# Optimization experiments

Measured on AMD Instinct MI355X. Metric: run time of the kernel, lower is better.

Reference implementation:

```python
import jax, jax.numpy as jnp
import numpy as np

EMBED_DIM = 1024
NUM_HEADS = 16
HEAD_DIM = EMBED_DIM // NUM_HEADS


def setup_inputs() -> dict:
    key = jax.random.key(0)
    ks = jax.random.split(key, 7)
    N, L = 2, 2048
    sv = 1.0 / np.sqrt(HEAD_DIM)
    so = 1.0 / np.sqrt(EMBED_DIM)
    return {
        "values": jax.random.normal(ks[0], (N, L, EMBED_DIM), jnp.float32),
        "keys": jax.random.normal(ks[1], (N, L, EMBED_DIM), jnp.float32),
        "query": jax.random.normal(ks[2], (N, L, EMBED_DIM), jnp.float32),
        # NOTE: original torch code applies self.values to v, k AND q; keys/queries
        # Linears are dead parameters, so only Wv/bv and fc_out are materialized.
        "Wv": jax.random.uniform(ks[3], (HEAD_DIM, HEAD_DIM), jnp.float32, -sv, sv),
        "bv": jax.random.uniform(ks[4], (HEAD_DIM,), jnp.float32, -sv, sv),
        "Wo": jax.random.uniform(ks[5], (EMBED_DIM, EMBED_DIM), jnp.float32, -so, so),
        "bo": jax.random.uniform(ks[6], (EMBED_DIM,), jnp.float32, -so, so),
    }


def reference(values, keys, query, Wv, bv, Wo, bo):
    N, Lq, _ = query.shape
    Lk = keys.shape[1]
    Lv = values.shape[1]
    # split heads: (N, L, H, D)
    v = values.reshape(N, Lv, NUM_HEADS, HEAD_DIM)
    k = keys.reshape(N, Lk, NUM_HEADS, HEAD_DIM)
    q = query.reshape(N, Lq, NUM_HEADS, HEAD_DIM)
    # faithful to source: the SAME value projection is applied to v, k, q
    proj = lambda x: jnp.einsum('nlhd,ed->nlhe', x, Wv) + bv
    v = proj(v)
    k = proj(k)
    q = proj(q)
    # energy: (N, H, Q, K); note scaling by sqrt(embed_dim), as in source
    energy = jnp.einsum('nqhd,nkhd->nhqk', q, k)
    attention = jax.nn.softmax(energy / jnp.sqrt(jnp.float32(EMBED_DIM)), axis=3)
    out = jnp.einsum('nhql,nlhd->nqhd', attention, v).reshape(N, Lq, EMBED_DIM)
    return out @ Wo.T + bo
```

## Files before the change

### kernel.cpp

```cpp
#include <hip/hip_runtime.h>

typedef unsigned short u16;
typedef __bf16 bf16x4 __attribute__((ext_vector_type(4)));
typedef __bf16 bf16x8 __attribute__((ext_vector_type(8)));
typedef float  f32x4  __attribute__((ext_vector_type(4)));
typedef float  f32x16 __attribute__((ext_vector_type(16)));

#define MFMA16(a, b, c) __builtin_amdgcn_mfma_f32_16x16x32_bf16((a), (b), (c), 0, 0, 0)
#define MFMA32(a, b, c) __builtin_amdgcn_mfma_f32_32x32x16_bf16((a), (b), (c), 0, 0, 0)


__global__ __launch_bounds__(256) void prep_kernel(
    const float* __restrict__ values, const float* __restrict__ keys,
    const float* __restrict__ query,  const float* __restrict__ Wv,
    const float* __restrict__ bv,     const float* __restrict__ Wo,
    u16* __restrict__ Qb, u16* __restrict__ Kb, u16* __restrict__ VTb,
    u16* __restrict__ Wob) {
    const int b = blockIdx.x;
    const int t = b >> 10;
    if (t == 3) {
        const int i = ((b - 3072) * 256 + threadIdx.x) * 4;
        float4 v = *(const float4*)&Wo[i];
        bf16x4 o = { (__bf16)v.x, (__bf16)v.y, (__bf16)v.z, (__bf16)v.w };
        *(bf16x4*)&Wob[i] = o;
        return;
    }
    __shared__ __align__(16) u16 Wvs[64 * 72];
    __shared__ __align__(16) u16 Xs[64 * 72];
    const int lt = b & 31, h = (b >> 5) & 15, n = (b >> 9) & 1;
    const int nh = n * 16 + h, l0 = lt * 64;
    const int tid = threadIdx.x, wave = tid >> 6, lane = tid & 63;
    const int quad = lane >> 4, l16 = lane & 15;
    const float* xin = (t == 0) ? values : (t == 1 ? keys : query);

#pragma unroll
    for (int j = 0; j < 4; ++j) {
        const int chunk = tid + 256 * j, r = chunk >> 4, c = (chunk & 15) * 4;
        float4 w = *(const float4*)&Wv[r * 64 + c];
        bf16x4 wb = { (__bf16)w.x, (__bf16)w.y, (__bf16)w.z, (__bf16)w.w };
        *(bf16x4*)&Wvs[r * 72 + c] = wb;
        float4 x = *(const float4*)&xin[(size_t)(n * 2048 + l0 + r) * 1024 + h * 64 + c];
        bf16x4 xb = { (__bf16)x.x, (__bf16)x.y, (__bf16)x.z, (__bf16)x.w };
        *(bf16x4*)&Xs[r * 72 + c] = xb;
    }
    __syncthreads();

    bf16x8 wf[4][2], xf[2];
#pragma unroll
    for (int f = 0; f < 4; ++f)
#pragma unroll
        for (int ks = 0; ks < 2; ++ks)
            wf[f][ks] = *(const bf16x8*)&Wvs[(f * 16 + l16) * 72 + ks * 32 + quad * 8];
#pragma unroll
    for (int ks = 0; ks < 2; ++ks)
        xf[ks] = *(const bf16x8*)&Xs[(wave * 16 + l16) * 72 + ks * 32 + quad * 8];

    f32x4 acc[4];
#pragma unroll
    for (int i = 0; i < 4; ++i) acc[i] = (f32x4){0.f, 0.f, 0.f, 0.f};

    if (t == 0) {
#pragma unroll
        for (int nf = 0; nf < 4; ++nf) {
            acc[nf] = MFMA16(xf[0], wf[nf][0], acc[nf]);
            acc[nf] = MFMA16(xf[1], wf[nf][1], acc[nf]);
        }
    } else {
#pragma unroll
        for (int mf = 0; mf < 4; ++mf) {
            acc[mf] = MFMA16(wf[mf][0], xf[0], acc[mf]);
            acc[mf] = MFMA16(wf[mf][1], xf[1], acc[mf]);
        }
    }
    __syncthreads();

    const float scale = (t == 2) ? 0.04508422f : 1.0f;
    if (t == 0) {
#pragma unroll
        for (int nf = 0; nf < 4; ++nf) {
            const float bias = bv[nf * 16 + l16];
            bf16x4 o = { (__bf16)(acc[nf][0] + bias), (__bf16)(acc[nf][1] + bias),
                         (__bf16)(acc[nf][2] + bias), (__bf16)(acc[nf][3] + bias) };
            *(bf16x4*)&Xs[(nf * 16 + l16) * 72 + wave * 16 + quad * 4] = o;
        }
    } else {
#pragma unroll
        for (int mf = 0; mf < 4; ++mf) {
            bf16x4 o = { (__bf16)((acc[mf][0] + bv[mf * 16 + quad * 4 + 0]) * scale),
                         (__bf16)((acc[mf][1] + bv[mf * 16 + quad * 4 + 1]) * scale),
                         (__bf16)((acc[mf][2] + bv[mf * 16 + quad * 4 + 2]) * scale),
                         (__bf16)((acc[mf][3] + bv[mf * 16 + quad * 4 + 3]) * scale) };
            *(bf16x4*)&Xs[(wave * 16 + l16) * 72 + mf * 16 + quad * 4] = o;
        }
    }
    __syncthreads();

    u16* dst = (t == 0) ? VTb : (t == 1 ? Kb : Qb);
#pragma unroll
    for (int j = 0; j < 2; ++j) {
        const int chunk = tid + 256 * j, r = chunk >> 3, c = (chunk & 7) * 8;
        const size_t off = (t == 0) ? (size_t)(nh * 64 + r) * 2048 + l0 + c
                                    : (size_t)(nh * 2048 + l0 + r) * 64 + c;
        *(int4*)&dst[off] = *(const int4*)&Xs[r * 72 + c];
    }
}

__global__ __launch_bounds__(256, 4) void flash_kernel(
    const u16* __restrict__ Qb, const u16* __restrict__ Kb,
    const u16* __restrict__ VTb, u16* __restrict__ Op,
    float* __restrict__ Lp) {
    __shared__ __align__(16) u16 Ks[64 * 72];
    __shared__ __align__(16) u16 Vs[64 * 72];
    __shared__ __align__(16) u16 Ps[4][32 * 72];
    const int b = blockIdx.x;
    const int nh = b >> 5, qsl = (b >> 1) & 15, ks = b & 1;
    const int tid = threadIdx.x, wave = tid >> 6, lane = tid & 63;
    const int l32 = lane & 31, half = lane >> 5;
    const int q0 = qsl * 128 + wave * 32;
    const int s4 = (b >> 1) * 4 + wave;
    u16* Pw = &Ps[wave][0];

    const u16* Qg = Qb + ((size_t)nh * 2048 + q0) * 64;
    bf16x8 qf[4];
#pragma unroll
    for (int kg = 0; kg < 4; ++kg)
        qf[kg] = *(const bf16x8*)&Qg[l32 * 64 + kg * 16 + half * 8];

    f32x16 Oacc[2];
#pragma unroll
    for (int dt = 0; dt < 2; ++dt)
#pragma unroll
        for (int r = 0; r < 16; ++r) Oacc[dt][r] = 0.f;
    float lsum = 0.f;

    const u16* Kg = Kb + (size_t)nh * 2048 * 64;
    const u16* Vg = VTb + (size_t)nh * 64 * 2048;

    for (int kt = 0; kt < 16; ++kt) {
        __syncthreads();
        const int k0 = ks * 1024 + kt * 64;
#pragma unroll
        for (int j = 0; j < 2; ++j) {
            const int chunk = tid + 256 * j, r = chunk >> 3, c = (chunk & 7) * 8;
            *(int4*)&Ks[r * 72 + c] = *(const int4*)&Kg[(size_t)(k0 + r) * 64 + c];
            *(int4*)&Vs[r * 72 + c] = *(const int4*)&Vg[(size_t)r * 2048 + k0 + c];
        }
        __syncthreads();

#pragma unroll
        for (int t2 = 0; t2 < 2; ++t2) {
            f32x16 s;
#pragma unroll
            for (int r = 0; r < 16; ++r) s[r] = 0.f;
#pragma unroll
            for (int kg = 0; kg < 4; ++kg) {
                bf16x8 ak = *(const bf16x8*)&Ks[(t2 * 32 + l32) * 72 + kg * 16 + half * 8];
                s = MFMA32(ak, qf[kg], s);
            }
#pragma unroll
            for (int a = 0; a < 4; ++a) {
                const float p0 = __builtin_amdgcn_exp2f(s[4 * a + 0]);
                const float p1 = __builtin_amdgcn_exp2f(s[4 * a + 1]);
                const float p2 = __builtin_amdgcn_exp2f(s[4 * a + 2]);
                const float p3 = __builtin_amdgcn_exp2f(s[4 * a + 3]);
                lsum += (p0 + p1) + (p2 + p3);
                bf16x4 pk = { (__bf16)p0, (__bf16)p1, (__bf16)p2, (__bf16)p3 };
                *(bf16x4*)&Pw[l32 * 72 + t2 * 32 + a * 8 + half * 4] = pk;
            }
        }

#pragma unroll
        for (int kk = 0; kk < 4; ++kk) {
            bf16x8 bp = *(const bf16x8*)&Pw[l32 * 72 + kk * 16 + half * 8];
#pragma unroll
            for (int dt = 0; dt < 2; ++dt) {
                bf16x8 av = *(const bf16x8*)&Vs[(dt * 32 + l32) * 72 + kk * 16 + half * 8];
                Oacc[dt] = MFMA32(av, bp, Oacc[dt]);
            }
        }
    }

    const float lq = lsum + __shfl_xor(lsum, 32);
    if (half == 0)
        Lp[((size_t)s4 * 2 + ks) * 32 + l32] = lq;

#pragma unroll
    for (int dt = 0; dt < 2; ++dt)
#pragma unroll
        for (int a = 0; a < 4; ++a) {
            bf16x4 o = { (__bf16)Oacc[dt][4 * a + 0], (__bf16)Oacc[dt][4 * a + 1],
                         (__bf16)Oacc[dt][4 * a + 2], (__bf16)Oacc[dt][4 * a + 3] };
            *(bf16x4*)&Pw[l32 * 72 + dt * 32 + a * 8 + half * 4] = o;
        }
    u16* Ob = Op + (size_t)ks * 4194304 +
              ((size_t)(nh >> 4) * 2048 + q0) * 1024 + (nh & 15) * 64;
#pragma unroll
    for (int j = 0; j < 4; ++j) {
        const int chunk = lane + 64 * j, r = chunk >> 3, c = (chunk & 7) * 8;
        *(int4*)&Ob[(size_t)r * 1024 + c] = *(const int4*)&Pw[r * 72 + c];
    }
}

__global__ __launch_bounds__(256) void combine_kernel(
    const u16* __restrict__ Op, const float* __restrict__ Lp,
    u16* __restrict__ AOb) {
    const int u = blockIdx.x * 256 + threadIdx.x;
    const int row = u >> 7, ecol = (u & 127) * 8;
    const int h = ecol >> 6;
    const int n = row >> 11, qsl = (row >> 7) & 15, w = (row >> 5) & 3, q = row & 31;
    const int s4 = (((n * 16 + h) * 16 + qsl) << 2) + w;
    const float l = Lp[(size_t)s4 * 2 * 32 + q] + Lp[((size_t)s4 * 2 + 1) * 32 + q];
    const float inv = 1.0f / l;
    const size_t off = (size_t)row * 1024 + ecol;
    bf16x8 a = *(const bf16x8*)&Op[off];
    bf16x8 c = *(const bf16x8*)&Op[4194304 + off];
    bf16x8 o;
#pragma unroll
    for (int i = 0; i < 8; ++i)
        o[i] = (__bf16)(((float)a[i] + (float)c[i]) * inv);
    *(bf16x8*)&AOb[off] = o;
}

__global__ __launch_bounds__(512) void out_gemm_kernel(
    const u16* __restrict__ A, const u16* __restrict__ Bw,
    const float* __restrict__ bo, float* __restrict__ out) {
    __shared__ __align__(16) u16 As[128 * 72];
    __shared__ __align__(16) u16 Bs[64 * 72];
    const int b = blockIdx.x, rt = b >> 4, ct = b & 15;
    const int row0 = rt * 128, col0 = ct * 64;
    const int tid = threadIdx.x, wave = tid >> 6, lane = tid & 63;
    const int l32 = lane & 31, half = lane >> 5;
    const int wr = wave & 3, wc = wave >> 2;

    f32x16 acc;
#pragma unroll
    for (int r = 0; r < 16; ++r) acc[r] = 0.f;

    for (int kt = 0; kt < 16; ++kt) {
        __syncthreads();
        const int k0 = kt * 64;
#pragma unroll
        for (int j = 0; j < 2; ++j) {
            const int chunk = tid + 512 * j, r = chunk >> 3, c = (chunk & 7) * 8;
            *(int4*)&As[r * 72 + c] = *(const int4*)&A[(size_t)(row0 + r) * 1024 + k0 + c];
        }
        {
            const int r = tid >> 3, c = (tid & 7) * 8;
            *(int4*)&Bs[r * 72 + c] = *(const int4*)&Bw[(size_t)(col0 + r) * 1024 + k0 + c];
        }
        __syncthreads();
#pragma unroll
        for (int kg = 0; kg < 4; ++kg) {
            bf16x8 af = *(const bf16x8*)&As[(wr * 32 + l32) * 72 + kg * 16 + half * 8];
            bf16x8 bf = *(const bf16x8*)&Bs[(wc * 32 + l32) * 72 + kg * 16 + half * 8];
            acc = MFMA32(af, bf, acc);
        }
    }

    const int col = col0 + wc * 32 + l32;
    const float bias = bo[col];
#pragma unroll
    for (int r = 0; r < 16; ++r) {
        const int row = row0 + wr * 32 + (r & 3) + 8 * (r >> 2) + 4 * half;
        out[(size_t)row * 1024 + col] = acc[r] + bias;
    }
}

extern "C" void kernel_launch(void* const* d_in, const int* in_sizes, int n_in,
                              void* d_out, int out_size, void* d_ws, size_t ws_size,
                              hipStream_t stream) {
    (void)in_sizes; (void)n_in; (void)out_size; (void)ws_size;
    const float* values = (const float*)d_in[0];
    const float* keys   = (const float*)d_in[1];
    const float* query  = (const float*)d_in[2];
    const float* Wv     = (const float*)d_in[3];
    const float* bv     = (const float*)d_in[4];
    const float* Wo     = (const float*)d_in[5];
    const float* bo     = (const float*)d_in[6];

    char* ws = (char*)d_ws;
    u16*   Qb  = (u16*)(ws);
    u16*   Kb  = (u16*)(ws + (8ull  << 20));
    u16*   VTb = (u16*)(ws + (16ull << 20));
    u16*   AOb = (u16*)(ws + (24ull << 20));
    u16*   Wob = (u16*)(ws + (32ull << 20));
    u16*   Op  = (u16*)(ws + (34ull << 20));
    float* Lp  = (float*)(ws + (50ull << 20));

    prep_kernel<<<4096, 256, 0, stream>>>(values, keys, query, Wv, bv, Wo,
                                          Qb, Kb, VTb, Wob);
    flash_kernel<<<1024, 256, 0, stream>>>(Qb, Kb, VTb, Op, Lp);
    combine_kernel<<<2048, 256, 0, stream>>>(Op, Lp, AOb);
    out_gemm_kernel<<<512, 512, 0, stream>>>(AOb, Wob, bo, (float*)d_out);
}
```

Baseline: 166.9 us.

## Quantize Q/K to FP8 for QK^T and fuse combine into output GEMM

```diff
diff --git a/kernel.cpp b/kernel.cpp
--- a/kernel.cpp
+++ b/kernel.cpp
@@ -1,20 +1,27 @@
 #include <hip/hip_runtime.h>
+#include <hip/hip_fp8.h>
 
 typedef unsigned short u16;
+typedef unsigned char  u8;
 typedef __bf16 bf16x4 __attribute__((ext_vector_type(4)));
 typedef __bf16 bf16x8 __attribute__((ext_vector_type(8)));
 typedef float  f32x4  __attribute__((ext_vector_type(4)));
 typedef float  f32x16 __attribute__((ext_vector_type(16)));
 
-#define MFMA16(a, b, c) __builtin_amdgcn_mfma_f32_16x16x32_bf16((a), (b), (c), 0, 0, 0)
-#define MFMA32(a, b, c) __builtin_amdgcn_mfma_f32_32x32x16_bf16((a), (b), (c), 0, 0, 0)
+#define MFMA16(a, b, c)   __builtin_amdgcn_mfma_f32_16x16x32_bf16((a), (b), (c), 0, 0, 0)
+#define MFMA32(a, b, c)   __builtin_amdgcn_mfma_f32_32x32x16_bf16((a), (b), (c), 0, 0, 0)
+#define MFMA32F8(a, b, c) __builtin_amdgcn_mfma_f32_32x32x16_fp8_fp8((a), (b), (c), 0, 0, 0)
+
+__device__ inline u8 to_e4m3(float f) {
+    return (u8)__hip_cvt_float_to_fp8(f, __HIP_SATFINITE, __HIP_E4M3);
+}
 
 
 __global__ __launch_bounds__(256) void prep_kernel(
     const float* __restrict__ values, const float* __restrict__ keys,
     const float* __restrict__ query,  const float* __restrict__ Wv,
     const float* __restrict__ bv,     const float* __restrict__ Wo,
-    u16* __restrict__ Qb, u16* __restrict__ Kb, u16* __restrict__ VTb,
+    u8* __restrict__ Qb, u8* __restrict__ Kb, u16* __restrict__ VTb,
     u16* __restrict__ Wob) {
     const int b = blockIdx.x;
     const int t = b >> 10;
@@ -27,6 +34,7 @@
     }
     __shared__ __align__(16) u16 Wvs[64 * 72];
     __shared__ __align__(16) u16 Xs[64 * 72];
+    u8* Xs8 = (u8*)Xs;
     const int lt = b & 31, h = (b >> 5) & 15, n = (b >> 9) & 1;
     const int nh = n * 16 + h, l0 = lt * 64;
     const int tid = threadIdx.x, wave = tid >> 6, lane = tid & 63;
@@ -74,7 +82,7 @@
     }
     __syncthreads();
 
-    const float scale = (t == 2) ? 0.04508422f : 1.0f;
+    const float scale = 0.2123305f;
     if (t == 0) {
 #pragma unroll
         for (int nf = 0; nf < 4; ++nf) {
@@ -86,30 +94,37 @@
     } else {
 #pragma unroll
         for (int mf = 0; mf < 4; ++mf) {
-            bf16x4 o = { (__bf16)((acc[mf][0] + bv[mf * 16 + quad * 4 + 0]) * scale),
-                         (__bf16)((acc[mf][1] + bv[mf * 16 + quad * 4 + 1]) * scale),
-                         (__bf16)((acc[mf][2] + bv[mf * 16 + quad * 4 + 2]) * scale),
-                         (__bf16)((acc[mf][3] + bv[mf * 16 + quad * 4 + 3]) * scale) };
-            *(bf16x4*)&Xs[(wave * 16 + l16) * 72 + mf * 16 + quad * 4] = o;
+            const u8 b0 = to_e4m3((acc[mf][0] + bv[mf * 16 + quad * 4 + 0]) * scale);
+            const u8 b1 = to_e4m3((acc[mf][1] + bv[mf * 16 + quad * 4 + 1]) * scale);
+            const u8 b2 = to_e4m3((acc[mf][2] + bv[mf * 16 + quad * 4 + 2]) * scale);
+            const u8 b3 = to_e4m3((acc[mf][3] + bv[mf * 16 + quad * 4 + 3]) * scale);
+            const int pk = (int)b0 | ((int)b1 << 8) | ((int)b2 << 16) | ((int)b3 << 24);
+            *(int*)&Xs8[(wave * 16 + l16) * 72 + mf * 16 + quad * 4] = pk;
         }
     }
     __syncthreads();
 
-    u16* dst = (t == 0) ? VTb : (t == 1 ? Kb : Qb);
-#pragma unroll
-    for (int j = 0; j < 2; ++j) {
-        const int chunk = tid + 256 * j, r = chunk >> 3, c = (chunk & 7) * 8;
-        const size_t off = (t == 0) ? (size_t)(nh * 64 + r) * 2048 + l0 + c
-                                    : (size_t)(nh * 2048 + l0 + r) * 64 + c;
-        *(int4*)&dst[off] = *(const int4*)&Xs[r * 72 + c];
+    if (t == 0) {
+#pragma unroll
+        for (int j = 0; j < 2; ++j) {
+            const int chunk = tid + 256 * j, r = chunk >> 3, c = (chunk & 7) * 8;
+            *(int4*)&VTb[(size_t)(nh * 64 + r) * 2048 + l0 + c] = *(const int4*)&Xs[r * 72 + c];
+        }
+    } else {
+        u8* dst = (t == 1) ? Kb : Qb;
+#pragma unroll
+        for (int j = 0; j < 2; ++j) {
+            const int chunk = tid + 256 * j, r = chunk >> 3, c = (chunk & 7) * 8;
+            *(int2*)&dst[(size_t)(nh * 2048 + l0 + r) * 64 + c] = *(const int2*)&Xs8[r * 72 + c];
+        }
     }
 }
 
 __global__ __launch_bounds__(256, 4) void flash_kernel(
-    const u16* __restrict__ Qb, const u16* __restrict__ Kb,
+    const u8* __restrict__ Qb, const u8* __restrict__ Kb,
     const u16* __restrict__ VTb, u16* __restrict__ Op,
     float* __restrict__ Lp) {
-    __shared__ __align__(16) u16 Ks[64 * 72];
+    __shared__ __align__(16) u8  Ks[64 * 72];
     __shared__ __align__(16) u16 Vs[64 * 72];
     __shared__ __align__(16) u16 Ps[4][32 * 72];
     const int b = blockIdx.x;
@@ -120,11 +135,11 @@
     const int s4 = (b >> 1) * 4 + wave;
     u16* Pw = &Ps[wave][0];
 
-    const u16* Qg = Qb + ((size_t)nh * 2048 + q0) * 64;
-    bf16x8 qf[4];
+    const u8* Qg = Qb + ((size_t)nh * 2048 + q0) * 64;
+    long qf[4];
 #pragma unroll
     for (int kg = 0; kg < 4; ++kg)
-        qf[kg] = *(const bf16x8*)&Qg[l32 * 64 + kg * 16 + half * 8];
+        qf[kg] = *(const long*)&Qg[l32 * 64 + kg * 16 + half * 8];
 
     f32x16 Oacc[2];
 #pragma unroll
@@ -133,7 +148,7 @@
         for (int r = 0; r < 16; ++r) Oacc[dt][r] = 0.f;
     float lsum = 0.f;
 
-    const u16* Kg = Kb + (size_t)nh * 2048 * 64;
+    const u8*  Kg = Kb + (size_t)nh * 2048 * 64;
     const u16* Vg = VTb + (size_t)nh * 64 * 2048;
 
     for (int kt = 0; kt < 16; ++kt) {
@@ -142,7 +157,7 @@
 #pragma unroll
         for (int j = 0; j < 2; ++j) {
             const int chunk = tid + 256 * j, r = chunk >> 3, c = (chunk & 7) * 8;
-            *(int4*)&Ks[r * 72 + c] = *(const int4*)&Kg[(size_t)(k0 + r) * 64 + c];
+            *(int2*)&Ks[r * 72 + c] = *(const int2*)&Kg[(size_t)(k0 + r) * 64 + c];
             *(int4*)&Vs[r * 72 + c] = *(const int4*)&Vg[(size_t)r * 2048 + k0 + c];
         }
         __syncthreads();
@@ -154,8 +169,8 @@
             for (int r = 0; r < 16; ++r) s[r] = 0.f;
 #pragma unroll
             for (int kg = 0; kg < 4; ++kg) {
-                bf16x8 ak = *(const bf16x8*)&Ks[(t2 * 32 + l32) * 72 + kg * 16 + half * 8];
-                s = MFMA32(ak, qf[kg], s);
+                long ak = *(const long*)&Ks[(t2 * 32 + l32) * 72 + kg * 16 + half * 8];
+                s = MFMA32F8(ak, qf[kg], s);
             }
 #pragma unroll
             for (int a = 0; a < 4; ++a) {
@@ -201,33 +216,15 @@
     }
 }
 
-__global__ __launch_bounds__(256) void combine_kernel(
+__global__ __launch_bounds__(512) void out_gemm_kernel(
     const u16* __restrict__ Op, const float* __restrict__ Lp,
-    u16* __restrict__ AOb) {
-    const int u = blockIdx.x * 256 + threadIdx.x;
-    const int row = u >> 7, ecol = (u & 127) * 8;
-    const int h = ecol >> 6;
-    const int n = row >> 11, qsl = (row >> 7) & 15, w = (row >> 5) & 3, q = row & 31;
-    const int s4 = (((n * 16 + h) * 16 + qsl) << 2) + w;
-    const float l = Lp[(size_t)s4 * 2 * 32 + q] + Lp[((size_t)s4 * 2 + 1) * 32 + q];
-    const float inv = 1.0f / l;
-    const size_t off = (size_t)row * 1024 + ecol;
-    bf16x8 a = *(const bf16x8*)&Op[off];
-    bf16x8 c = *(const bf16x8*)&Op[4194304 + off];
-    bf16x8 o;
-#pragma unroll
-    for (int i = 0; i < 8; ++i)
-        o[i] = (__bf16)(((float)a[i] + (float)c[i]) * inv);
-    *(bf16x8*)&AOb[off] = o;
-}
-
-__global__ __launch_bounds__(512) void out_gemm_kernel(
-    const u16* __restrict__ A, const u16* __restrict__ Bw,
-    const float* __restrict__ bo, float* __restrict__ out) {
+    const u16* __restrict__ Bw, const float* __restrict__ bo,
+    float* __restrict__ out) {
     __shared__ __align__(16) u16 As[128 * 72];
     __shared__ __align__(16) u16 Bs[64 * 72];
     const int b = blockIdx.x, rt = b >> 4, ct = b & 15;
     const int row0 = rt * 128, col0 = ct * 64;
+    const int n16 = (rt >> 4) * 16, qsl = rt & 15;
     const int tid = threadIdx.x, wave = tid >> 6, lane = tid & 63;
     const int l32 = lane & 31, half = lane >> 5;
     const int wr = wave & 3, wc = wave >> 2;
@@ -239,10 +236,22 @@
     for (int kt = 0; kt < 16; ++kt) {
         __syncthreads();
         const int k0 = kt * 64;
+        const int s4h = ((n16 + kt) * 16 + qsl) * 4;
 #pragma unroll
         for (int j = 0; j < 2; ++j) {
             const int chunk = tid + 512 * j, r = chunk >> 3, c = (chunk & 7) * 8;
-            *(int4*)&As[r * 72 + c] = *(const int4*)&A[(size_t)(row0 + r) * 1024 + k0 + c];
+            const int w = r >> 5, q = r & 31;
+            const float l = Lp[(size_t)(s4h + w) * 64 + q] +
+                            Lp[(size_t)(s4h + w) * 64 + 32 + q];
+            const float inv = 1.0f / l;
+            const size_t off = (size_t)(row0 + r) * 1024 + k0 + c;
+            bf16x8 a = *(const bf16x8*)&Op[off];
+            bf16x8 c8 = *(const bf16x8*)&Op[4194304 + off];
+            bf16x8 o;
+#pragma unroll
+            for (int i = 0; i < 8; ++i)
+                o[i] = (__bf16)(((float)a[i] + (float)c8[i]) * inv);
+            *(bf16x8*)&As[r * 72 + c] = o;
         }
         {
             const int r = tid >> 3, c = (tid & 7) * 8;
@@ -279,17 +288,15 @@
     const float* bo     = (const float*)d_in[6];
 
     char* ws = (char*)d_ws;
-    u16*   Qb  = (u16*)(ws);
-    u16*   Kb  = (u16*)(ws + (8ull  << 20));
-    u16*   VTb = (u16*)(ws + (16ull << 20));
-    u16*   AOb = (u16*)(ws + (24ull << 20));
-    u16*   Wob = (u16*)(ws + (32ull << 20));
-    u16*   Op  = (u16*)(ws + (34ull << 20));
-    float* Lp  = (float*)(ws + (50ull << 20));
+    u8*    Qb  = (u8*)(ws);
+    u8*    Kb  = (u8*)(ws + (4ull  << 20));
+    u16*   VTb = (u16*)(ws + (8ull  << 20));
+    u16*   Wob = (u16*)(ws + (16ull << 20));
+    u16*   Op  = (u16*)(ws + (18ull << 20));
+    float* Lp  = (float*)(ws + (34ull << 20));
 
     prep_kernel<<<4096, 256, 0, stream>>>(values, keys, query, Wv, bv, Wo,
                                           Qb, Kb, VTb, Wob);
     flash_kernel<<<1024, 256, 0, stream>>>(Qb, Kb, VTb, Op, Lp);
-    combine_kernel<<<2048, 256, 0, stream>>>(Op, Lp, AOb);
-    out_gemm_kernel<<<512, 512, 0, stream>>>(AOb, Wob, bo, (float*)d_out);
-}
+    out_gemm_kernel<<<512, 512, 0, stream>>>(Op, Lp, Wob, bo, (float*)d_out);
+}
```

Result: slower. 175.1 us (+4.9%).
